# Performance work log

Hardware: AMD Instinct MI355X
Metric: run time of the kernel (lower is better)

The kernel has to match this reference:

```python
import jax, jax.numpy as jnp
import numpy as np

B, N, D, H = 128, 2000, 128, 8
HD = D // H  # head_dim = 16
CLIP = 10.0


def setup_inputs() -> dict:
    key = jax.random.key(0)
    ks = jax.random.split(key, 20)
    s = 0.05
    w = lambda k, sh: jax.random.normal(k, sh, jnp.float32) * s
    return {
        "embeddings": jax.random.normal(ks[0], (B, N, D), jnp.float32),
        "context": jax.random.normal(ks[1], (B, D), jnp.float32),
        "step_context": jax.random.normal(ks[2], (B, 1, D + 1), jnp.float32),
        "mask": jax.random.randint(ks[3], (B, 1, N), 0, 2).astype(bool),
        "Wq_c": w(ks[4], (D, D)), "bq_c": w(ks[5], (D,)),
        "Wq_s": w(ks[6], (D, D + 1)), "bq_s": w(ks[7], (D,)),
        "Wk": w(ks[8], (D, D)), "bk": w(ks[9], (D,)),
        "Wkt": w(ks[10], (D, D)), "bkt": w(ks[11], (D,)),
        "Wv": w(ks[12], (D, D)), "bv": w(ks[13], (D,)),
        "Wo": w(ks[14], (D, D)), "bo": w(ks[15], (D,)),
    }


def _heads(x):
    # (B, S, D) -> (B, H, S, HD)
    return x.reshape(x.shape[0], x.shape[1], H, HD).transpose(0, 2, 1, 3)


def reference(embeddings, context, step_context, mask,
              Wq_c, bq_c, Wq_s, bq_s, Wk, bk, Wkt, bkt, Wv, bv, Wo, bo):
    # get_projections
    K = _heads(embeddings @ Wk.T + bk)        # (B, H, N, HD)
    V = _heads(embeddings @ Wv.T + bv)        # (B, H, N, HD)
    K_tanh = embeddings @ Wkt.T + bkt         # (B, N, D)
    Q_context = context[:, None, :] @ Wq_c.T + bq_c     # (B, 1, D)
    Q_step = step_context @ Wq_s.T + bq_s                # (B, 1, D)
    Q = _heads(Q_context + Q_step)            # (B, H, 1, HD)

    # decoder_mha: matmul -> mask(-inf) -> softmax -> mask(0) -> matmul -> w_out
    compat = jnp.einsum('bhqd,bhkd->bhqk', Q, K) / jnp.sqrt(jnp.float32(HD))
    m4 = mask[:, None, :, :]                  # (B, 1, 1, N) broadcast over heads
    compat = jnp.where(m4, -jnp.inf, compat)
    attn_w = jax.nn.softmax(compat, axis=-1)
    attn_w = jnp.where(m4, 0.0, attn_w)
    attn = jnp.einsum('bhqk,bhkd->bhqd', attn_w, V)      # (B, H, 1, HD)
    mha = attn.transpose(0, 2, 1, 3).reshape(B, -1, D) @ Wo.T + bo  # (B, 1, D)

    # get_log_p: matmul -> mask(-inf) -> log_softmax
    # NOTE: the original computes tanh(compat)*clip into `x` but never uses it
    # (dead code) -- replicated faithfully by omitting the clip.
    logits = jnp.einsum('bqd,bkd->bqk', mha, K_tanh) / jnp.sqrt(jnp.float32(D))
    logits = jnp.where(mask, -jnp.inf, logits)
    return jax.nn.log_softmax(logits, axis=-1)  # (B, 1, N)
```

## Files before the change

kernel.cpp:

```cpp
#include <hip/hip_runtime.h>
#include <cstdint>
#include <cstddef>
#include <math.h>

#define B 128
#define N 2000
#define D 128
#define H 8
#define HD 16
#define NCA 16
#define TPCA 125
#define NCL 16
#define TPCL 125
#define NEG_BIG (-1.0e30f)

#define DOT4(e, w) ((e).x*(w).x + (e).y*(w).y + (e).z*(w).z + (e).w*(w).w)

__global__ __launch_bounds__(128) void k_prep(
    const float* __restrict__ ctx, const float* __restrict__ sctx,
    const float* __restrict__ Wq_c, const float* __restrict__ bq_c,
    const float* __restrict__ Wq_s, const float* __restrict__ bq_s,
    const float* __restrict__ Wk,   const float* __restrict__ bk,
    float* __restrict__ wq, float* __restrict__ cq)
{
    int b = blockIdx.x, t = threadIdx.x;
    __shared__ float4 c14[D / 4];
    __shared__ float c2s[D + 1], Qs[D];
    if (t < D / 4) c14[t] = reinterpret_cast<const float4*>(ctx + b * D)[t];
    c2s[t] = sctx[b * (D + 1) + t];
    if (t == 0) c2s[D] = sctx[b * (D + 1) + D];
    __syncthreads();
    float q = bq_c[t] + bq_s[t];
    const float4* wc4 = reinterpret_cast<const float4*>(Wq_c + t * D);
    #pragma unroll 8
    for (int j = 0; j < D / 4; j++) {
        float4 w = wc4[j], c = c14[j];
        q += w.x * c.x + w.y * c.y + w.z * c.z + w.w * c.w;
    }
    const float* wsr = Wq_s + t * (D + 1);
    #pragma unroll 8
    for (int j = 0; j < D + 1; j++) q += wsr[j] * c2s[j];
    Qs[t] = q;
    __syncthreads();
    float acc[H] = {};
    #pragma unroll
    for (int r = 0; r < D; r++)
        acc[r >> 4] += Wk[r * D + t] * Qs[r];
    #pragma unroll
    for (int h = 0; h < H; h++) wq[b * (H * D) + h * D + t] = acc[h] * 0.25f;
    if (t < H) {
        float c = 0.f;
        #pragma unroll
        for (int i = 0; i < HD; i++) c += Qs[t * HD + i] * bk[t * HD + i];
        cq[b * H + t] = c * 0.25f;
    }
}

__global__ __launch_bounds__(256, 8) void k_attn(
    const float* __restrict__ emb, const unsigned char* __restrict__ mask,
    const float* __restrict__ wq, const float* __restrict__ cq,
    float* __restrict__ pl, float* __restrict__ ps)
{
    int b = blockIdx.y, c = blockIdx.x, t = threadIdx.x;
    int n0 = c * TPCA;

    __shared__ __align__(16) float shmem[4096];
    __shared__ float cqs_s[H];
    __shared__ float redl[8][4];

    float4* wqs   = reinterpret_cast<float4*>(shmem);
    float4* plds4 = reinterpret_cast<float4*>(shmem + 1024);

    wqs[t] = reinterpret_cast<const float4*>(wq + b * (H * D))[t];
    if (t < H) cqs_s[t] = cq[b * H + t];
    __syncthreads();

    const float4* e4 = reinterpret_cast<const float4*>(emb + (size_t)b * N * D);

    {
        int qtok = t >> 2, qp = t & 3;
        bool live1 = (qtok + 64 < TPCA);
        int r1 = live1 ? (qtok + 64) : 0;
        const float4* er0 = e4 + (size_t)(n0 + qtok) * 32;
        const float4* er1 = e4 + (size_t)(n0 + r1) * 32;
        float a0[H] = {}, a1[H] = {};
        #pragma unroll
        for (int j = 0; j < 8; j++) {
            int o = j * 4 + qp;
            float4 e0 = er0[o], e1 = er1[o];
            #pragma unroll
            for (int h = 0; h < H; h++) {
                float4 w = wqs[h * 32 + o];
                a0[h] += DOT4(e0, w);
                a1[h] += DOT4(e1, w);
            }
        }
        #pragma unroll
        for (int h = 0; h < H; h++) {
            a0[h] += __shfl_xor(a0[h], 1); a0[h] += __shfl_xor(a0[h], 2);
            a1[h] += __shfl_xor(a1[h], 1); a1[h] += __shfl_xor(a1[h], 2);
        }
        if (qp == 0) {
            const unsigned char* mrow = mask + (size_t)b * N + n0;
            bool d0 = mrow[qtok] != 0;
            bool d1 = !live1 || (mrow[r1] != 0);
            float4 pa, pb;
            #define EMIT(ACC, DEAD, TOK) \
                pa.x = (DEAD) ? 0.f : __expf(ACC[0] + cqs_s[0]); \
                pa.y = (DEAD) ? 0.f : __expf(ACC[1] + cqs_s[1]); \
                pa.z = (DEAD) ? 0.f : __expf(ACC[2] + cqs_s[2]); \
                pa.w = (DEAD) ? 0.f : __expf(ACC[3] + cqs_s[3]); \
                pb.x = (DEAD) ? 0.f : __expf(ACC[4] + cqs_s[4]); \
                pb.y = (DEAD) ? 0.f : __expf(ACC[5] + cqs_s[5]); \
                pb.z = (DEAD) ? 0.f : __expf(ACC[6] + cqs_s[6]); \
                pb.w = (DEAD) ? 0.f : __expf(ACC[7] + cqs_s[7]); \
                plds4[(TOK) * 3] = pa; plds4[(TOK) * 3 + 1] = pb;
            EMIT(a0, d0, qtok)
            if (live1) { EMIT(a1, d1, qtok + 64) }
            #undef EMIT
        }
    }
    __syncthreads();

    int grp = t >> 5, gl = t & 31;
    int half = grp & 1;
    int tset = grp >> 1;
    float4 a[4];
    float  La[4];
    #pragma unroll
    for (int h = 0; h < 4; h++) { a[h] = {0.f, 0.f, 0.f, 0.f}; La[h] = 0.f; }
    for (int i = tset; i < TPCA; i += 4) {
        float4 p = plds4[i * 3 + half];
        if (p.x != 0.f || p.y != 0.f || p.z != 0.f || p.w != 0.f) {
            float4 e = e4[(size_t)(n0 + i) * 32 + gl];
            a[0].x += p.x * e.x; a[0].y += p.x * e.y; a[0].z += p.x * e.z; a[0].w += p.x * e.w;
            a[1].x += p.y * e.x; a[1].y += p.y * e.y; a[1].z += p.y * e.z; a[1].w += p.y * e.w;
            a[2].x += p.z * e.x; a[2].y += p.z * e.y; a[2].z += p.z * e.z; a[2].w += p.z * e.w;
            a[3].x += p.w * e.x; a[3].y += p.w * e.y; a[3].z += p.w * e.z; a[3].w += p.w * e.w;
            La[0] += p.x; La[1] += p.y; La[2] += p.z; La[3] += p.w;
        }
    }
    __syncthreads();

    float4* reds = reinterpret_cast<float4*>(shmem);
    #pragma unroll
    for (int h = 0; h < 4; h++) reds[(grp * 4 + h) * 32 + gl] = a[h];
    if (gl == 0) {
        #pragma unroll
        for (int h = 0; h < 4; h++) redl[grp][h] = La[h];
    }
    __syncthreads();

    {
        int hh = t >> 5, dd = gl;
        int hf = hh >> 2, hl = hh & 3;
        float4 r = {0.f, 0.f, 0.f, 0.f};
        #pragma unroll
        for (int ts = 0; ts < 4; ts++) {
            float4 x = reds[((ts * 2 + hf) * 4 + hl) * 32 + dd];
            r.x += x.x; r.y += x.y; r.z += x.z; r.w += x.w;
        }
        reinterpret_cast<float4*>(ps + (((size_t)(b * NCA + c)) * H + hh) * D)[dd] = r;
        if (t < H) {
            int hf2 = t >> 2, hl2 = t & 3;
            float L = 0.f;
            #pragma unroll
            for (int ts = 0; ts < 4; ts++) L += redl[ts * 2 + hf2][hl2];
            pl[(b * NCA + c) * H + t] = L;
        }
    }
}

__global__ __launch_bounds__(128) void k_comb(
    const float* __restrict__ pl, const float* __restrict__ ps,
    const float* __restrict__ Wv, const float* __restrict__ bv,
    const float* __restrict__ Wo, const float* __restrict__ bo,
    const float* __restrict__ Wkt, const float* __restrict__ bkt,
    float* __restrict__ g, float* __restrict__ c2)
{
    int b = blockIdx.x, t = threadIdx.x;
    __shared__ float invLs[H];
    __shared__ float s_s[H][D + 4];
    __shared__ float attn_s[D];
    __shared__ float mha_s[D];
    if (t < H) {
        float L = 0.f;
        #pragma unroll
        for (int c = 0; c < NCA; c++) L += pl[(b * NCA + c) * H + t];
        invLs[t] = 1.0f / L;
    }
    __syncthreads();
    #pragma unroll
    for (int h = 0; h < H; h++) {
        float v = 0.f;
        #pragma unroll
        for (int c = 0; c < NCA; c++)
            v += ps[(((size_t)(b * NCA + c)) * H + h) * D + t];
        s_s[h][t] = v * invLs[h];
    }
    __syncthreads();
    {
        int h = t >> 4;
        const float* wr = Wv + t * D;
        float a = bv[t];
        #pragma unroll 8
        for (int d = 0; d < D; d++) a += wr[d] * s_s[h][d];
        attn_s[t] = a;
    }
    __syncthreads();
    {
        const float* wr = Wo + t * D;
        float m = bo[t];
        #pragma unroll 8
        for (int r = 0; r < D; r++) m += wr[r] * attn_s[r];
        mha_s[t] = m;
    }
    __syncthreads();
    {
        float gv = 0.f;
        #pragma unroll 8
        for (int d = 0; d < D; d++) gv += Wkt[d * D + t] * mha_s[d];
        g[b * D + t] = gv * 0.08838834764831845f;
    }
    if (t == 0) {
        float c = 0.f;
        #pragma unroll 8
        for (int d = 0; d < D; d++) c += mha_s[d] * bkt[d];
        c2[b] = c * 0.08838834764831845f;
    }
}

__global__ __launch_bounds__(256) void k_logits(
    const float* __restrict__ emb, const unsigned char* __restrict__ mask,
    const float* __restrict__ g, const float* __restrict__ c2,
    float* __restrict__ out)
{
    int b = blockIdx.y, t = threadIdx.x;
    int qtok = t >> 2, qp = t & 3;
    __shared__ float4 gs[D / 4];
    __shared__ float c2s;
    if (t < D / 4) gs[t] = reinterpret_cast<const float4*>(g + b * D)[t];
    if (t == 0) c2s = c2[b];
    __syncthreads();
    int n0 = blockIdx.x * TPCL;
    const float4* e4 = reinterpret_cast<const float4*>(emb + (size_t)b * N * D);
    #pragma unroll
    for (int k = 0; k < 2; k++) {
        int ng = k * 64 + qtok;
        bool live = (ng < TPCL);
        int nr = live ? (n0 + ng) : n0;
        bool m = !live || (mask[(size_t)b * N + nr] != 0);
        float acc = 0.f;
        if (!m) {
            const float4* erow = e4 + (size_t)nr * 32;
            #pragma unroll
            for (int j = 0; j < 8; j++) {
                float4 e = erow[j * 4 + qp];
                float4 w = gs[j * 4 + qp];
                acc += e.x * w.x + e.y * w.y + e.z * w.z + e.w * w.w;
            }
        }
        acc += __shfl_xor(acc, 1);
        acc += __shfl_xor(acc, 2);
        if (live && qp == 0)
            out[(size_t)b * N + nr] = m ? -INFINITY : (acc + c2s);
    }
}

__global__ __launch_bounds__(256) void k_lsm(float* __restrict__ out)
{
    __shared__ float red[4];
    int t = threadIdx.x;
    float* row = out + (size_t)blockIdx.x * N;
    float v[8];
    float mx = -INFINITY;
    #pragma unroll
    for (int i = 0; i < 8; i++) {
        int idx = t + i * 256;
        v[i] = (idx < N) ? row[idx] : -INFINITY;
        mx = fmaxf(mx, v[i]);
    }
    #pragma unroll
    for (int o = 32; o; o >>= 1) mx = fmaxf(mx, __shfl_xor(mx, o));
    if ((t & 63) == 0) red[t >> 6] = mx;
    __syncthreads();
    mx = fmaxf(fmaxf(red[0], red[1]), fmaxf(red[2], red[3]));
    __syncthreads();
    float s = 0.f;
    #pragma unroll
    for (int i = 0; i < 8; i++)
        if (v[i] != -INFINITY) s += __expf(v[i] - mx);
    #pragma unroll
    for (int o = 32; o; o >>= 1) s += __shfl_xor(s, o);
    if ((t & 63) == 0) red[t >> 6] = s;
    __syncthreads();
    s = red[0] + red[1] + red[2] + red[3];
    float lse = mx + logf(s);
    #pragma unroll
    for (int i = 0; i < 8; i++) {
        int idx = t + i * 256;
        if (idx < N) row[idx] = (v[i] == -INFINITY) ? NEG_BIG : (v[i] - lse);
    }
}

extern "C" void kernel_launch(void* const* d_in, const int* in_sizes, int n_in,
                              void* d_out, int out_size, void* d_ws, size_t ws_size,
                              hipStream_t stream)
{
    const float* emb  = (const float*)d_in[0];
    const float* ctx  = (const float*)d_in[1];
    const float* sctx = (const float*)d_in[2];
    const unsigned char* mask = (const unsigned char*)d_in[3];
    const float* Wq_c = (const float*)d_in[4];
    const float* bq_c = (const float*)d_in[5];
    const float* Wq_s = (const float*)d_in[6];
    const float* bq_s = (const float*)d_in[7];
    const float* Wk   = (const float*)d_in[8];
    const float* bk   = (const float*)d_in[9];
    const float* Wkt  = (const float*)d_in[10];
    const float* bkt  = (const float*)d_in[11];
    const float* Wv   = (const float*)d_in[12];
    const float* bv   = (const float*)d_in[13];
    const float* Wo   = (const float*)d_in[14];
    const float* bo   = (const float*)d_in[15];
    float* out = (float*)d_out;

    float* ws = (float*)d_ws;
    float* wq = ws;
    float* cq = ws + 131072;
    float* pl = ws + 132096;
    float* ps = ws + 148480;
    float* g  = ws + 2245632;
    float* c2 = ws + 2262016;

    k_prep  <<<dim3(B), dim3(128), 0, stream>>>(ctx, sctx, Wq_c, bq_c, Wq_s, bq_s, Wk, bk, wq, cq);
    k_attn  <<<dim3(NCA, B), dim3(256), 0, stream>>>(emb, mask, wq, cq, pl, ps);
    k_comb  <<<dim3(B), dim3(128), 0, stream>>>(pl, ps, Wv, bv, Wo, bo, Wkt, bkt, g, c2);
    k_logits<<<dim3(NCL, B), dim3(256), 0, stream>>>(emb, mask, g, c2, out);
    k_lsm   <<<dim3(B), dim3(256), 0, stream>>>(out);
}
```

Measured before the change: 98.69 us.

## Split attention kernel into compat and weighted-sum kernels via global buffer

The fused attention kernel is split in two. One kernel computes exp scores per token and head and writes them to a global scratch buffer. A second kernel, launched with half as many chunks of twice the tokens, reads those scores and accumulates the weighted embedding sums. This is meant to remove the intra-block sync between phases and to halve the partial sums the combine kernel must reduce. In exchange it adds a kernel launch, a global round trip for the probabilities, and a second full read of the embeddings for live tokens.

```diff
diff --git a/kernel.cpp b/kernel.cpp
--- a/kernel.cpp
+++ b/kernel.cpp
@@ -8,8 +8,10 @@
 #define D 128
 #define H 8
 #define HD 16
-#define NCA 16
-#define TPCA 125
+#define NCC 16
+#define TPCC 125
+#define NCW 8
+#define TPW 250
 #define NCL 16
 #define TPCL 125
 #define NEG_BIG (-1.0e30f)
@@ -56,20 +58,16 @@
     }
 }
 
-__global__ __launch_bounds__(256, 8) void k_attn(
+__global__ __launch_bounds__(256, 8) void k_compat(
     const float* __restrict__ emb, const unsigned char* __restrict__ mask,
     const float* __restrict__ wq, const float* __restrict__ cq,
-    float* __restrict__ pl, float* __restrict__ ps)
+    float* __restrict__ p)
 {
     int b = blockIdx.y, c = blockIdx.x, t = threadIdx.x;
-    int n0 = c * TPCA;
-
-    __shared__ __align__(16) float shmem[4096];
+    int n0 = c * TPCC;
+
+    __shared__ __align__(16) float4 wqs[256];
     __shared__ float cqs_s[H];
-    __shared__ float redl[8][4];
-
-    float4* wqs   = reinterpret_cast<float4*>(shmem);
-    float4* plds4 = reinterpret_cast<float4*>(shmem + 1024);
 
     wqs[t] = reinterpret_cast<const float4*>(wq + b * (H * D))[t];
     if (t < H) cqs_s[t] = cq[b * H + t];
@@ -77,72 +75,83 @@
 
     const float4* e4 = reinterpret_cast<const float4*>(emb + (size_t)b * N * D);
 
-    {
-        int qtok = t >> 2, qp = t & 3;
-        bool live1 = (qtok + 64 < TPCA);
-        int r1 = live1 ? (qtok + 64) : 0;
-        const float4* er0 = e4 + (size_t)(n0 + qtok) * 32;
-        const float4* er1 = e4 + (size_t)(n0 + r1) * 32;
-        float a0[H] = {}, a1[H] = {};
-        #pragma unroll
-        for (int j = 0; j < 8; j++) {
-            int o = j * 4 + qp;
-            float4 e0 = er0[o], e1 = er1[o];
-            #pragma unroll
-            for (int h = 0; h < H; h++) {
-                float4 w = wqs[h * 32 + o];
-                a0[h] += DOT4(e0, w);
-                a1[h] += DOT4(e1, w);
-            }
-        }
+    int qtok = t >> 2, qp = t & 3;
+    bool live1 = (qtok + 64 < TPCC);
+    int r1 = live1 ? (qtok + 64) : 0;
+    const float4* er0 = e4 + (size_t)(n0 + qtok) * 32;
+    const float4* er1 = e4 + (size_t)(n0 + r1) * 32;
+    float a0[H] = {}, a1[H] = {};
+    #pragma unroll
+    for (int j = 0; j < 8; j++) {
+        int o = j * 4 + qp;
+        float4 e0 = er0[o], e1 = er1[o];
         #pragma unroll
         for (int h = 0; h < H; h++) {
-            a0[h] += __shfl_xor(a0[h], 1); a0[h] += __shfl_xor(a0[h], 2);
-            a1[h] += __shfl_xor(a1[h], 1); a1[h] += __shfl_xor(a1[h], 2);
-        }
-        if (qp == 0) {
-            const unsigned char* mrow = mask + (size_t)b * N + n0;
-            bool d0 = mrow[qtok] != 0;
-            bool d1 = !live1 || (mrow[r1] != 0);
-            float4 pa, pb;
-            #define EMIT(ACC, DEAD, TOK) \
-                pa.x = (DEAD) ? 0.f : __expf(ACC[0] + cqs_s[0]); \
-                pa.y = (DEAD) ? 0.f : __expf(ACC[1] + cqs_s[1]); \
-                pa.z = (DEAD) ? 0.f : __expf(ACC[2] + cqs_s[2]); \
-                pa.w = (DEAD) ? 0.f : __expf(ACC[3] + cqs_s[3]); \
-                pb.x = (DEAD) ? 0.f : __expf(ACC[4] + cqs_s[4]); \
-                pb.y = (DEAD) ? 0.f : __expf(ACC[5] + cqs_s[5]); \
-                pb.z = (DEAD) ? 0.f : __expf(ACC[6] + cqs_s[6]); \
-                pb.w = (DEAD) ? 0.f : __expf(ACC[7] + cqs_s[7]); \
-                plds4[(TOK) * 3] = pa; plds4[(TOK) * 3 + 1] = pb;
-            EMIT(a0, d0, qtok)
-            if (live1) { EMIT(a1, d1, qtok + 64) }
-            #undef EMIT
-        }
-    }
-    __syncthreads();
-
+            float4 w = wqs[h * 32 + o];
+            a0[h] += DOT4(e0, w);
+            a1[h] += DOT4(e1, w);
+        }
+    }
+    #pragma unroll
+    for (int h = 0; h < H; h++) {
+        a0[h] += __shfl_xor(a0[h], 1); a0[h] += __shfl_xor(a0[h], 2);
+        a1[h] += __shfl_xor(a1[h], 1); a1[h] += __shfl_xor(a1[h], 2);
+    }
+    if (qp == 0) {
+        const unsigned char* mrow = mask + (size_t)b * N + n0;
+        bool d0 = mrow[qtok] != 0;
+        bool d1 = !live1 || (mrow[r1] != 0);
+        float4* pg = reinterpret_cast<float4*>(p) + ((size_t)b * N + n0) * 2;
+        float4 pa, pb;
+        #define EMIT(ACC, DEAD, TOK) \
+            pa.x = (DEAD) ? 0.f : __expf(ACC[0] + cqs_s[0]); \
+            pa.y = (DEAD) ? 0.f : __expf(ACC[1] + cqs_s[1]); \
+            pa.z = (DEAD) ? 0.f : __expf(ACC[2] + cqs_s[2]); \
+            pa.w = (DEAD) ? 0.f : __expf(ACC[3] + cqs_s[3]); \
+            pb.x = (DEAD) ? 0.f : __expf(ACC[4] + cqs_s[4]); \
+            pb.y = (DEAD) ? 0.f : __expf(ACC[5] + cqs_s[5]); \
+            pb.z = (DEAD) ? 0.f : __expf(ACC[6] + cqs_s[6]); \
+            pb.w = (DEAD) ? 0.f : __expf(ACC[7] + cqs_s[7]); \
+            pg[(TOK) * 2] = pa; pg[(TOK) * 2 + 1] = pb;
+        EMIT(a0, d0, qtok)
+        if (live1) { EMIT(a1, d1, qtok + 64) }
+        #undef EMIT
+    }
+}
+
+__global__ __launch_bounds__(256, 8) void k_wsum(
+    const float* __restrict__ emb, const float* __restrict__ p,
+    float* __restrict__ pl, float* __restrict__ ps)
+{
+    int b = blockIdx.y, c = blockIdx.x, t = threadIdx.x;
+    int n0 = c * TPW;
     int grp = t >> 5, gl = t & 31;
     int half = grp & 1;
     int tset = grp >> 1;
+
+    __shared__ __align__(16) float4 reds[8 * 4 * 32];
+    __shared__ float redl[8][4];
+
+    const float4* e4 = reinterpret_cast<const float4*>(emb + (size_t)b * N * D);
+    const float4* pg = reinterpret_cast<const float4*>(p) + ((size_t)b * N + n0) * 2 + half;
+
     float4 a[4];
     float  La[4];
     #pragma unroll
     for (int h = 0; h < 4; h++) { a[h] = {0.f, 0.f, 0.f, 0.f}; La[h] = 0.f; }
-    for (int i = tset; i < TPCA; i += 4) {
-        float4 p = plds4[i * 3 + half];
-        if (p.x != 0.f || p.y != 0.f || p.z != 0.f || p.w != 0.f) {
+    #pragma unroll 2
+    for (int i = tset; i < TPW; i += 4) {
+        float4 pv = pg[i * 2];
+        if (pv.x != 0.f || pv.y != 0.f || pv.z != 0.f || pv.w != 0.f) {
             float4 e = e4[(size_t)(n0 + i) * 32 + gl];
-            a[0].x += p.x * e.x; a[0].y += p.x * e.y; a[0].z += p.x * e.z; a[0].w += p.x * e.w;
-            a[1].x += p.y * e.x; a[1].y += p.y * e.y; a[1].z += p.y * e.z; a[1].w += p.y * e.w;
-            a[2].x += p.z * e.x; a[2].y += p.z * e.y; a[2].z += p.z * e.z; a[2].w += p.z * e.w;
-            a[3].x += p.w * e.x; a[3].y += p.w * e.y; a[3].z += p.w * e.z; a[3].w += p.w * e.w;
-            La[0] += p.x; La[1] += p.y; La[2] += p.z; La[3] += p.w;
-        }
-    }
-    __syncthreads();
-
-    float4* reds = reinterpret_cast<float4*>(shmem);
+            a[0].x += pv.x * e.x; a[0].y += pv.x * e.y; a[0].z += pv.x * e.z; a[0].w += pv.x * e.w;
+            a[1].x += pv.y * e.x; a[1].y += pv.y * e.y; a[1].z += pv.y * e.z; a[1].w += pv.y * e.w;
+            a[2].x += pv.z * e.x; a[2].y += pv.z * e.y; a[2].z += pv.z * e.z; a[2].w += pv.z * e.w;
+            a[3].x += pv.w * e.x; a[3].y += pv.w * e.y; a[3].z += pv.w * e.z; a[3].w += pv.w * e.w;
+            La[0] += pv.x; La[1] += pv.y; La[2] += pv.z; La[3] += pv.w;
+        }
+    }
+
     #pragma unroll
     for (int h = 0; h < 4; h++) reds[(grp * 4 + h) * 32 + gl] = a[h];
     if (gl == 0) {
@@ -160,13 +169,13 @@
             float4 x = reds[((ts * 2 + hf) * 4 + hl) * 32 + dd];
             r.x += x.x; r.y += x.y; r.z += x.z; r.w += x.w;
         }
-        reinterpret_cast<float4*>(ps + (((size_t)(b * NCA + c)) * H + hh) * D)[dd] = r;
+        reinterpret_cast<float4*>(ps + (((size_t)(b * NCW + c)) * H + hh) * D)[dd] = r;
         if (t < H) {
             int hf2 = t >> 2, hl2 = t & 3;
             float L = 0.f;
             #pragma unroll
             for (int ts = 0; ts < 4; ts++) L += redl[ts * 2 + hf2][hl2];
-            pl[(b * NCA + c) * H + t] = L;
+            pl[(b * NCW + c) * H + t] = L;
         }
     }
 }
@@ -186,7 +195,7 @@
     if (t < H) {
         float L = 0.f;
         #pragma unroll
-        for (int c = 0; c < NCA; c++) L += pl[(b * NCA + c) * H + t];
+        for (int c = 0; c < NCW; c++) L += pl[(b * NCW + c) * H + t];
         invLs[t] = 1.0f / L;
     }
     __syncthreads();
@@ -194,8 +203,8 @@
     for (int h = 0; h < H; h++) {
         float v = 0.f;
         #pragma unroll
-        for (int c = 0; c < NCA; c++)
-            v += ps[(((size_t)(b * NCA + c)) * H + h) * D + t];
+        for (int c = 0; c < NCW; c++)
+            v += ps[(((size_t)(b * NCW + c)) * H + h) * D + t];
         s_s[h][t] = v * invLs[h];
     }
     __syncthreads();
@@ -328,13 +337,15 @@
     float* ws = (float*)d_ws;
     float* wq = ws;
     float* cq = ws + 131072;
-    float* pl = ws + 132096;
-    float* ps = ws + 148480;
-    float* g  = ws + 2245632;
-    float* c2 = ws + 2262016;
+    float* p  = ws + 132096;
+    float* pl = ws + 2180096;
+    float* ps = ws + 2188288;
+    float* g  = ws + 3236864;
+    float* c2 = ws + 3253248;
 
     k_prep  <<<dim3(B), dim3(128), 0, stream>>>(ctx, sctx, Wq_c, bq_c, Wq_s, bq_s, Wk, bk, wq, cq);
-    k_attn  <<<dim3(NCA, B), dim3(256), 0, stream>>>(emb, mask, wq, cq, pl, ps);
+    k_compat<<<dim3(NCC, B), dim3(256), 0, stream>>>(emb, mask, wq, cq, p);
+    k_wsum  <<<dim3(NCW, B), dim3(256), 0, stream>>>(emb, p, pl, ps);
     k_comb  <<<dim3(B), dim3(128), 0, stream>>>(pl, ps, Wv, bv, Wo, bo, Wkt, bkt, g, c2);
     k_logits<<<dim3(NCL, B), dim3(256), 0, stream>>>(emb, mask, g, c2, out);
     k_lsm   <<<dim3(B), dim3(256), 0, stream>>>(out);
```

New measurement: 123.9 us. 25.6% more time.
